# Kernel tuning notes

Measured on AMD Instinct MI355X. Metric: run time of the kernel, lower is better.

The kernel has to match this reference:

```python
import jax, jax.numpy as jnp
import numpy as np

jax.config.update("jax_enable_x64", True)

B, N, M_EQ, D_INEQ = 64, 128, 32, 64
RHO = 1.0
THRES = 1e-5
MAX_ITERS = 5000  # safety cap (original loops until relative objective change <= 1e-5)


def setup_inputs() -> dict:
    key = jax.random.key(0)
    kL, kq, kG, kA, kx0, ks = jax.random.split(key, 6)
    L = jax.random.normal(kL, (B, N, N))
    Q = jnp.einsum('bij,bkj->bik', L, L) / N + jnp.eye(N)  # SPD, well-conditioned
    q = jax.random.normal(kq, (B, N))
    G = jax.random.normal(kG, (B, D_INEQ, N))
    A = jax.random.normal(kA, (B, M_EQ, N))
    x0 = jax.random.normal(kx0, (B, N))
    slack = jax.random.uniform(ks, (B, D_INEQ)) + 0.1
    h = jnp.einsum('bdn,bn->bd', G, x0) + slack  # strictly feasible ineq
    b = jnp.einsum('bmn,bn->bm', A, x0)          # feasible eq
    f32 = jnp.float32
    return {"Q": Q.astype(f32), "q": q.astype(f32), "G": G.astype(f32),
            "h": h.astype(f32), "A": A.astype(f32), "b": b.astype(f32)}


def _alt_diff_batch(Q, q, G, h, A, b):
    """Batched Alt-Diff ADMM QP solve; returns (x [B,n], dx/dq [B,n,n])."""
    Bb, n = q.shape
    d = h.shape[1]
    m = b.shape[1]
    dt = Q.dtype
    AtA = jnp.einsum('bmi,bmj->bij', A, A)
    GtG = jnp.einsum('bdi,bdj->bij', G, G)
    R = -jnp.linalg.inv(Q + RHO * AtA + RHO * GtG)
    ATb = RHO * jnp.einsum('bmn,bm->bn', A, b)
    GTh = RHO * jnp.einsum('bdn,bd->bn', G, h)
    eye = jnp.eye(n, dtype=dt)

    def obj(x):
        return 0.5 * jnp.einsum('bi,bij,bj->b', x, Q, x) + jnp.einsum('bi,bi->b', q, x)

    init = dict(
        xk=jnp.zeros((Bb, n), dt), sk=jnp.zeros((Bb, d), dt),
        lamb=jnp.zeros((Bb, m), dt), nu=jnp.zeros((Bb, d), dt),
        dxk=jnp.zeros((Bb, n, n), dt), dsk=jnp.zeros((Bb, d, n), dt),
        dlamb=jnp.zeros((Bb, m, n), dt), dnu=jnp.zeros((Bb, d, n), dt),
        res_prev=jnp.full((Bb,), 1000.0, dt),   # res = [1000, -100] init
        res_cur=jnp.full((Bb,), -100.0, dt),
        done=jnp.zeros((Bb,), bool),
        it=jnp.zeros((), jnp.int32),
    )

    def cond(s):
        return jnp.logical_and(jnp.any(~s["done"]), s["it"] < MAX_ITERS)

    def body(s):
        xk = jnp.einsum('bij,bj->bi', R,
                        q + jnp.einsum('bmn,bm->bn', A, s["lamb"])
                          + jnp.einsum('bdn,bd->bn', G, s["nu"]) - ATb
                          + RHO * jnp.einsum('bdn,bd->bn', G, s["sk"]) - GTh)
        dxk = jnp.einsum('bij,bjk->bik', R,
                         eye + jnp.einsum('bmn,bmk->bnk', A, s["dlamb"])
                             + jnp.einsum('bdn,bdk->bnk', G, s["dnu"])
                             + RHO * jnp.einsum('bdn,bdk->bnk', G, s["dsk"]))
        Gx = jnp.einsum('bdn,bn->bd', G, xk)
        sk = jax.nn.relu(-(1.0 / RHO) * s["nu"] - (Gx - h))
        sgn = (sk > 0).astype(dt)  # sgn applied to already-relu'd sk, as in source
        dsk = (-1.0 / RHO) * sgn[:, :, None] * (s["dnu"] + RHO * jnp.einsum('bdn,bnk->bdk', G, dxk))
        lamb = s["lamb"] + RHO * (jnp.einsum('bmn,bn->bm', A, xk) - b)
        dlamb = s["dlamb"] + RHO * jnp.einsum('bmn,bnk->bmk', A, dxk)
        nu = s["nu"] + RHO * (Gx + sk - h)
        dnu = s["dnu"] + RHO * (jnp.einsum('bdn,bnk->bdk', G, dxk) + dsk)
        res_new = obj(xk)

        keep = s["done"]

        def sel(old, new):
            mask = keep.reshape((-1,) + (1,) * (new.ndim - 1))
            return jnp.where(mask, old, new)

        res_prev = jnp.where(keep, s["res_prev"], s["res_cur"])
        res_cur = jnp.where(keep, s["res_cur"], res_new)
        done = keep | (jnp.abs((res_cur - res_prev) / res_prev) <= THRES)
        return dict(
            xk=sel(s["xk"], xk), sk=sel(s["sk"], sk),
            lamb=sel(s["lamb"], lamb), nu=sel(s["nu"], nu),
            dxk=sel(s["dxk"], dxk), dsk=sel(s["dsk"], dsk),
            dlamb=sel(s["dlamb"], dlamb), dnu=sel(s["dnu"], dnu),
            res_prev=res_prev, res_cur=res_cur, done=done, it=s["it"] + 1,
        )

    final = jax.lax.while_loop(cond, body, init)
    return final["xk"], final["dxk"]


def reference(Q, q, G, h, A, b):
    out_dtype = q.dtype
    f64 = jnp.float64
    x, _dx = _alt_diff_batch(Q.astype(f64), q.astype(f64), G.astype(f64),
                             h.astype(f64), A.astype(f64), b.astype(f64))
    return x.astype(out_dtype)
```

## Files before the change

### kernel.cpp

```cpp
#include <hip/hip_runtime.h>

#define NN 128
#define ME 32
#define DI 64
#define NZ 96
#define ROWD 130
#define MAXIT 5000

#define OFF_UN 16640
#define ROWB  (OFF_UN)
#define COLB  (OFF_UN + 256)
#define FPLO  (2*OFF_UN)
#define FPHI  (2*OFF_UN + 512)
#define TV0   (OFF_UN + 384)
#define TV1   (OFF_UN + 512)
#define FLG   (OFF_UN + 544)
#define YBUF  (OFF_UN)
#define KBUF  (OFF_UN + 1536)
#define CPART (OFF_UN + 1024)
#define VP    (OFF_UN + 1280)
#define BASEV (OFF_UN + 1792)
#define QBV   (OFF_UN + 1888)
#define FPART (OFF_UN + 1024)
#define RHSV  (OFF_UN + 1280)
#define XPART (OFF_UN + 1408)
#define CB    (OFF_UN + 2688)
#define QBUF  (OFF_UN + 2816)
#define V1    (OFF_UN + 2944)
#define V2    (OFF_UN + 3072)
#define HB    (OFF_UN + 3200)
#define BB    (OFF_UN + 3264)
#define CST   (OFF_UN + 3296)
#define ZBF   (OFF_UN + 3304)
#define LDS_DBL (OFF_UN + 3400)

typedef __attribute__((ext_vector_type(2))) float f32x2;

__device__ __forceinline__ float rlf(float v, int lane) {
  return __uint_as_float((unsigned)__builtin_amdgcn_readlane((int)__float_as_uint(v), lane));
}
__device__ __forceinline__ f32x2 fma2(f32x2 a, f32x2 b, f32x2 c) {
  return __builtin_elementwise_fma(a, b, c);
}

__global__ __launch_bounds__(256, 1) void altdiff_kernel(
    const float* __restrict__ Qg, const float* __restrict__ qg,
    const float* __restrict__ Gg, const float* __restrict__ hg,
    const float* __restrict__ Ag, const float* __restrict__ bg,
    float* __restrict__ out)
{
  extern __shared__ double ldsd[];
  float* const ldsf = (float*)ldsd;

  const int bidx = blockIdx.x;
  const int tid  = threadIdx.x;
  const int w    = tid >> 6;
  const int l    = tid & 63;
  const int lm   = l & 31;
  const int ia   = tid & 127;
  const int hh   = tid >> 7;

  const float* Qb = Qg + (size_t)bidx * NN * NN;
  const float* Ab = Ag + (size_t)bidx * ME * NN;
  const float* Gb = Gg + (size_t)bidx * DI * NN;
  const float* qb = qg + (size_t)bidx * NN;
  const float* hb = hg + (size_t)bidx * DI;
  const float* bv = bg + (size_t)bidx * ME;

  if (tid < DI) ldsd[HB + tid] = (double)hb[tid];
  else if (tid < DI + ME) ldsd[BB + tid - DI] = (double)bv[tid - DI];
  if (tid >= 128) ldsd[QBUF + tid - 128] = (double)qb[tid - 128];

  const int r = tid >> 4, c = tid & 15;
  double acc[8][8];

  {
    const float4* Q4 = (const float4*)Qb;
#pragma unroll
    for (int rr = 0; rr < 8; ++rr) {
      float4 q0 = Q4[((8*r+rr) << 5) + 2*c];
      float4 q1 = Q4[((8*r+rr) << 5) + 2*c + 1];
      acc[rr][0]=(double)q0.x; acc[rr][1]=(double)q0.y; acc[rr][2]=(double)q0.z; acc[rr][3]=(double)q0.w;
      acc[rr][4]=(double)q1.x; acc[rr][5]=(double)q1.y; acc[rr][6]=(double)q1.z; acc[rr][7]=(double)q1.w;
    }
    const float4* A4 = (const float4*)Ab;
    for (int m = 0; m < ME; ++m) {
      float4 u0 = A4[(m << 5) + 2*r], u1 = A4[(m << 5) + 2*r + 1];
      float4 v0 = A4[(m << 5) + 2*c], v1 = A4[(m << 5) + 2*c + 1];
      double uu[8] = {(double)u0.x,(double)u0.y,(double)u0.z,(double)u0.w,
                      (double)u1.x,(double)u1.y,(double)u1.z,(double)u1.w};
      double vv[8] = {(double)v0.x,(double)v0.y,(double)v0.z,(double)v0.w,
                      (double)v1.x,(double)v1.y,(double)v1.z,(double)v1.w};
#pragma unroll
      for (int rr = 0; rr < 8; ++rr)
#pragma unroll
        for (int cc = 0; cc < 8; ++cc)
          acc[rr][cc] = fma(uu[rr], vv[cc], acc[rr][cc]);
    }
    const float4* G4 = (const float4*)Gb;
    for (int d = 0; d < DI; ++d) {
      float4 u0 = G4[(d << 5) + 2*r], u1 = G4[(d << 5) + 2*r + 1];
      float4 v0 = G4[(d << 5) + 2*c], v1 = G4[(d << 5) + 2*c + 1];
      double uu[8] = {(double)u0.x,(double)u0.y,(double)u0.z,(double)u0.w,
                      (double)u1.x,(double)u1.y,(double)u1.z,(double)u1.w};
      double vv[8] = {(double)v0.x,(double)v0.y,(double)v0.z,(double)v0.w,
                      (double)v1.x,(double)v1.y,(double)v1.z,(double)v1.w};
#pragma unroll
      for (int rr = 0; rr < 8; ++rr)
#pragma unroll
        for (int cc = 0; cc < 8; ++cc)
          acc[rr][cc] = fma(uu[rr], vv[cc], acc[rr][cc]);
    }
  }

  {
    if (r == 0) {
#pragma unroll
      for (int cc = 0; cc < 8; ++cc) ldsd[ROWB + 8*c + cc] = acc[0][cc];
    }
    if (c == 0) {
#pragma unroll
      for (int rr = 0; rr < 8; ++rr) ldsd[COLB + 8*r + rr] = acc[rr][0];
    }
    __syncthreads();
    for (int k = 0; k < NN; ++k) {
      const int pb = (k & 1) << 7;
      const int krt = k >> 3, kcl = k & 7;
      double rowk[8], colv[8];
#pragma unroll
      for (int cc = 0; cc < 8; ++cc) rowk[cc] = ldsd[ROWB + pb + 8*c + cc];
#pragma unroll
      for (int rr = 0; rr < 8; ++rr) colv[rr] = ldsd[COLB + pb + 8*r + rr];
      const double dkk  = ldsd[ROWB + pb + k];
      const double rcpd = 1.0 / dkk;
      double rdv[8];
#pragma unroll
      for (int cc = 0; cc < 8; ++cc) rdv[cc] = rowk[cc] * rcpd;
      const bool pivR = (r == krt), pivC = (c == krt);
#pragma unroll
      for (int rr = 0; rr < 8; ++rr) {
        const double cv = colv[rr] * rcpd;
        const bool pr = pivR && (rr == kcl);
#pragma unroll
        for (int cc = 0; cc < 8; ++cc) {
          double gen = fma(-cv, rowk[cc], acc[rr][cc]);
          acc[rr][cc] = pr ? rdv[cc] : gen;
        }
      }
      if (pivC) {
#pragma unroll
        for (int cc = 0; cc < 8; ++cc) if (cc == kcl) {
#pragma unroll
          for (int rr = 0; rr < 8; ++rr) {
            const bool pr2 = pivR && (rr == kcl);
            acc[rr][cc] = pr2 ? -rcpd : colv[rr] * rcpd;
          }
        }
      }
      if (k < NN - 1) {
        const int pb2 = ((k + 1) & 1) << 7;
        const int krt2 = (k + 1) >> 3, kcl2 = (k + 1) & 7;
        if (r == krt2) {
#pragma unroll
          for (int rr = 0; rr < 8; ++rr) if (rr == kcl2) {
#pragma unroll
            for (int cc = 0; cc < 8; ++cc) ldsd[ROWB + pb2 + 8*c + cc] = acc[rr][cc];
          }
        }
        if (c == krt2) {
#pragma unroll
          for (int cc = 0; cc < 8; ++cc) if (cc == kcl2) {
#pragma unroll
            for (int rr = 0; rr < 8; ++rr) ldsd[COLB + pb2 + 8*r + rr] = acc[rr][cc];
          }
        }
      }
      __syncthreads();
    }
#pragma unroll
    for (int rr = 0; rr < 8; ++rr) {
      double2* dst = (double2*)(ldsd + (8*r+rr)*ROWD + 8*c);
#pragma unroll
      for (int t = 0; t < 4; ++t) dst[t] = make_double2(acc[rr][2*t], acc[rr][2*t+1]);
    }
  }
  __syncthreads();

  f32x2 Kp[12], Kp2[12];
  for (int blk = 0; blk < 8; ++blk) {
    {
      const float* gp[6];
#pragma unroll
      for (int jj = 0; jj < 6; ++jj) {
        int it = 12*blk + 6*hh + jj;
        gp[jj] = (it < DI) ? (Gb + it*NN) : (Ab + (it - DI)*NN);
      }
      double a2[6] = {0,0,0,0,0,0};
#pragma unroll 4
      for (int t = 0; t < NN; ++t) {
        double rv = ldsd[t*ROWD + ia];
#pragma unroll
        for (int jj = 0; jj < 6; ++jj)
          a2[jj] = fma(rv, (double)gp[jj][t], a2[jj]);
      }
      double2* yst = (double2*)(ldsd + YBUF + ia*12 + 6*hh);
#pragma unroll
      for (int p = 0; p < 3; ++p) yst[p] = make_double2(a2[2*p], a2[2*p+1]);
    }
    __syncthreads();
    {
      const int r2 = (ia < NZ) ? ia : 0;
      const float* brow = (r2 < DI) ? (Gb + r2*NN) : (Ab + (r2 - DI)*NN);
      double a2[6] = {0,0,0,0,0,0};
#pragma unroll 4
      for (int t = 0; t < NN; ++t) {
        double bvv = (double)brow[t];
        const double2* yr = (const double2*)(ldsd + YBUF + t*12 + 6*hh);
        double2 y0 = yr[0], y1 = yr[1], y2 = yr[2];
        a2[0] = fma(bvv, y0.x, a2[0]); a2[1] = fma(bvv, y0.y, a2[1]);
        a2[2] = fma(bvv, y1.x, a2[2]); a2[3] = fma(bvv, y1.y, a2[3]);
        a2[4] = fma(bvv, y2.x, a2[4]); a2[5] = fma(bvv, y2.y, a2[5]);
      }
      if (ia < NZ) {
#pragma unroll
        for (int jj = 0; jj < 6; ++jj) ldsd[KBUF + (6*hh + jj)*NZ + ia] = a2[jj];
      }
    }
    __syncthreads();
    if (w == (blk >> 1)) {
      if ((blk & 1) == 0) {
#pragma unroll
        for (int p = 0; p < 6; ++p) {
          Kp [p].x = (float)ldsd[KBUF + (2*p  )*NZ + l];
          Kp [p].y = (float)ldsd[KBUF + (2*p+1)*NZ + l];
          Kp2[p].x = (float)ldsd[KBUF + (2*p  )*NZ + 64 + lm];
          Kp2[p].y = (float)ldsd[KBUF + (2*p+1)*NZ + 64 + lm];
        }
      } else {
#pragma unroll
        for (int p = 0; p < 6; ++p) {
          Kp [6+p].x = (float)ldsd[KBUF + (2*p  )*NZ + l];
          Kp [6+p].y = (float)ldsd[KBUF + (2*p+1)*NZ + l];
          Kp2[6+p].x = (float)ldsd[KBUF + (2*p  )*NZ + 64 + lm];
          Kp2[6+p].y = (float)ldsd[KBUF + (2*p+1)*NZ + 64 + lm];
        }
      }
    }
    __syncthreads();
  }

  {
    double s = 0;
#pragma unroll 8
    for (int jc = 0; jc < 48; ++jc) {
      int j = 48*hh + jc;
      double coef = (j < DI) ? ldsd[HB + j] : ldsd[BB + j - DI];
      const float* src = (j < DI) ? (Gb + j*NN) : (Ab + (j - DI)*NN);
      s = fma(-(double)src[ia], coef, s);
    }
    ldsd[CPART + hh*128 + ia] = s;
  }
  __syncthreads();
  if (tid < NN) ldsd[CB + tid] = ldsd[QBUF + tid] + ldsd[CPART + tid] + ldsd[CPART + 128 + tid];
  __syncthreads();

  {
    double a = 0, b2 = 0;
#pragma unroll 4
    for (int tt = 0; tt < 64; ++tt) {
      int t = 64*hh + tt;
      double rv = ldsd[t*ROWD + ia];
      a  = fma(rv, ldsd[CB + t], a);
      b2 = fma(rv, ldsd[QBUF + t], b2);
    }
    ldsd[VP + hh*128 + ia] = a;
    ldsd[VP + 256 + hh*128 + ia] = b2;
  }
  __syncthreads();
  if (tid < NN) {
    ldsd[V1 + tid] = ldsd[VP + tid] + ldsd[VP + 128 + tid];
    ldsd[V2 + tid] = ldsd[VP + 256 + tid] + ldsd[VP + 384 + tid];
  }
  __syncthreads();

  {
    const int r2 = (ia < NZ) ? ia : 0;
    const float* brow = (r2 < DI) ? (Gb + r2*NN) : (Ab + (r2 - DI)*NN);
    const int voff = hh ? V2 : V1;
    double s = 0;
#pragma unroll 4
    for (int t = 0; t < NN; ++t) s = fma((double)brow[t], ldsd[voff + t], s);
    if (ia < NZ) ldsd[(hh ? QBV : BASEV) + ia] = s;
  }
  if (w == 0) {
    double pc = ldsd[V1+l]*ldsd[CB+l]   + ldsd[V1+64+l]*ldsd[CB+64+l];
    double pq = ldsd[V1+l]*ldsd[QBUF+l] + ldsd[V1+64+l]*ldsd[QBUF+64+l];
#pragma unroll
    for (int off = 32; off >= 1; off >>= 1) { pc += __shfl_xor(pc, off); pq += __shfl_xor(pq, off); }
    if (l == 0) { ldsd[CST] = pc; ldsd[CST+1] = pq; }
  }
  __syncthreads();

  const double h_r   = ldsd[HB + l];
  const double b_r   = ldsd[BB + lm];
  const double baseA = ldsd[BASEV + l];
  const double baseB = ldsd[BASEV + 64 + lm];
  const double qvA   = ldsd[QBV + l];
  const double qvB   = ldsd[QBV + 64 + lm];
  const double S_uc  = ldsd[CST], S_qu = ldsd[CST + 1];
  double nu = 0.0, lam = 0.0;
  double zlo = 0.0, zhi = 0.0;
  double zAlo = 0.0, zAhi = 0.0, zBlo = 0.0, zBhi = 0.0, zClo = 0.0, zChi = 0.0;
  double res_prev = 1000.0, res_cur = -100.0;

  {
    ldsf[FPLO + 4*l + (w ^ (l & 3))] = 0.f;
    if (l < 32) ldsf[FPHI + 4*lm + (w ^ (lm & 3))] = 0.f;
    if (tid == 0) { ldsd[FLG] = 0.0; ldsd[FLG + 1] = 0.0; }
  }

  for (int it = 0; it < MAXIT + 3; ++it) {
    __syncthreads();
    const int pf  = (it & 1) << 8;
    const int phf = (it & 1) << 7;
    const int bprev = (it + 1) & 1;
    double fl = ldsd[FLG + bprev];
    float4 plo = {0.f, 0.f, 0.f, 0.f}, phi4 = {0.f, 0.f, 0.f, 0.f};
    if (w != 3) plo  = *(const float4*)&ldsf[FPLO + pf  + 4*l];
    if (w >= 2) phi4 = *(const float4*)&ldsf[FPHI + phf + 4*lm];
    double t1v[16];
    if (w == 1) {
      const double2* tp = (const double2*)(ldsd + TV1 + bprev*16);
#pragma unroll
      for (int u = 0; u < 8; ++u) { double2 v = tp[u]; t1v[2*u] = v.x; t1v[2*u+1] = v.y; }
    }
    double a40 = 0, a41 = 0, a42 = 0, a43 = 0;
    if (w == 3) {
      const int g = l & 15;
      const double* tb = ldsd + TV0 + bprev*64;
      a40 = tb[g]; a41 = tb[g + 16]; a42 = tb[g + 32]; a43 = tb[g + 48];
    }
    double ylo = 0.0, yhi = 0.0;
    if (w != 3) ylo = (double)((plo.x + plo.y) + (plo.z + plo.w)) + baseA;
    if (w >= 2) yhi = (double)((phi4.x + phi4.y) + (phi4.z + phi4.w)) + baseB;
    if (it >= 3 && fl != 0.0) break;
    if (w == 2) { zClo = zBlo; zChi = zBhi; zBlo = zAlo; zBhi = zAhi; zAlo = zlo; zAhi = zhi; }
    if (it < MAXIT) {
      float zflo = 0.f, zfhi = 0.f;
      if (w != 3) {
        double t  = (h_r - nu) - ylo;
        double sk = fmax(t, 0.0);
        nu  = sk - t;
        zlo = nu + sk;
        zflo = (float)zlo;
      }
      if (w >= 2) {
        lam = lam + yhi - b_r;
        zhi = lam;
        zfhi = (float)zhi;
      }
      if (w == 2) {
        double tv = fma(qvA, zAlo, -0.5*(zAlo*(baseA + ylo) + ylo*ylo));
        tv += (l < 32) ? fma(qvB, zAhi, -0.5*(zAhi*(baseB + yhi) + yhi*yhi)) : 0.0;
        ldsd[TV0 + (it & 1)*64 + l] = tv;
      }
      f32x2 A0 = {0.f, 0.f}, A1 = A0, B0 = A0, B1 = A0;
      if (w == 0) {
#pragma unroll
        for (int p = 0; p < 12; p += 2) {
          f32x2 z0 = {rlf(zflo, 2*p),     rlf(zflo, 2*p + 1)};
          A0 = fma2(Kp[p],   z0, A0); B0 = fma2(Kp2[p],   z0, B0);
          f32x2 z1 = {rlf(zflo, 2*p + 2), rlf(zflo, 2*p + 3)};
          A1 = fma2(Kp[p+1], z1, A1); B1 = fma2(Kp2[p+1], z1, B1);
        }
      } else if (w == 1) {
#pragma unroll
        for (int p = 0; p < 12; p += 2) {
          f32x2 z0 = {rlf(zflo, 24 + 2*p),     rlf(zflo, 24 + 2*p + 1)};
          A0 = fma2(Kp[p],   z0, A0); B0 = fma2(Kp2[p],   z0, B0);
          f32x2 z1 = {rlf(zflo, 24 + 2*p + 2), rlf(zflo, 24 + 2*p + 3)};
          A1 = fma2(Kp[p+1], z1, A1); B1 = fma2(Kp2[p+1], z1, B1);
        }
      } else if (w == 2) {
#pragma unroll
        for (int p = 0; p < 8; p += 2) {
          f32x2 z0 = {rlf(zflo, 48 + 2*p),     rlf(zflo, 48 + 2*p + 1)};
          A0 = fma2(Kp[p],   z0, A0); B0 = fma2(Kp2[p],   z0, B0);
          f32x2 z1 = {rlf(zflo, 48 + 2*p + 2), rlf(zflo, 48 + 2*p + 3)};
          A1 = fma2(Kp[p+1], z1, A1); B1 = fma2(Kp2[p+1], z1, B1);
        }
#pragma unroll
        for (int p = 8; p < 12; p += 2) {
          f32x2 z0 = {rlf(zfhi, 2*(p-8)),     rlf(zfhi, 2*(p-8) + 1)};
          A0 = fma2(Kp[p],   z0, A0); B0 = fma2(Kp2[p],   z0, B0);
          f32x2 z1 = {rlf(zfhi, 2*(p-7)),     rlf(zfhi, 2*(p-7) + 1)};
          A1 = fma2(Kp[p+1], z1, A1); B1 = fma2(Kp2[p+1], z1, B1);
        }
      } else {
#pragma unroll
        for (int p = 0; p < 12; p += 2) {
          f32x2 z0 = {rlf(zfhi, 8 + 2*p),     rlf(zfhi, 8 + 2*p + 1)};
          A0 = fma2(Kp[p],   z0, A0); B0 = fma2(Kp2[p],   z0, B0);
          f32x2 z1 = {rlf(zfhi, 8 + 2*p + 2), rlf(zfhi, 8 + 2*p + 3)};
          A1 = fma2(Kp[p+1], z1, A1); B1 = fma2(Kp2[p+1], z1, B1);
        }
      }
      f32x2 As = A0 + A1, Bs = B0 + B1;
      float pa0 = As.x + As.y;
      float pa1 = Bs.x + Bs.y;
      ldsf[FPLO + (pf ^ 256) + 4*l + (w ^ (l & 3))] = pa0;
      if (l < 32) ldsf[FPHI + (phf ^ 128) + 4*lm + (w ^ (lm & 3))] = pa1;
    }
    if (w == 3 && l < 16 && it >= 1 && it <= MAXIT)
      ldsd[TV1 + (it & 1)*16 + l] = (a40 + a41) + (a42 + a43);
    if (w == 1 && it >= 2 && it <= MAXIT + 1) {
      double s1 = ((t1v[0] + t1v[1]) + (t1v[2] + t1v[3])) + ((t1v[4] + t1v[5]) + (t1v[6] + t1v[7]));
      double s2 = ((t1v[8] + t1v[9]) + (t1v[10] + t1v[11])) + ((t1v[12] + t1v[13]) + (t1v[14] + t1v[15]));
      double obj = (s1 + s2) - 0.5*S_uc + S_qu;
      res_prev = res_cur; res_cur = obj;
      if (l == 0)
        ldsd[FLG + (it & 1)] = (fabs(res_cur - res_prev) <= 1e-5 * fabs(res_prev)) ? 1.0 : 0.0;
    }
  }

  if (w == 2) {
    ldsd[ZBF + l] = zClo;
    if (l < 32) ldsd[ZBF + 64 + l] = zChi;
  }
  __syncthreads();
  {
    double s = 0;
#pragma unroll 8
    for (int jc = 0; jc < 48; ++jc) {
      int j = 48*hh + jc;
      double zj = ldsd[ZBF + j];
      const float* src = (j < DI) ? (Gb + j*NN) : (Ab + (j - DI)*NN);
      s = fma((double)src[ia], zj, s);
    }
    ldsd[FPART + hh*128 + ia] = s;
  }
  __syncthreads();
  if (tid < NN) ldsd[RHSV + tid] = ldsd[CB + tid] + ldsd[FPART + tid] + ldsd[FPART + 128 + tid];
  __syncthreads();
  {
    double s = 0;
#pragma unroll 4
    for (int tt = 0; tt < 64; ++tt) {
      int t = 64*hh + tt;
      s = fma(ldsd[t*ROWD + ia], ldsd[RHSV + t], s);
    }
    ldsd[XPART + hh*128 + ia] = s;
  }
  __syncthreads();
  if (tid < NN)
    out[(size_t)bidx * NN + tid] = (float)(ldsd[XPART + tid] + ldsd[XPART + 128 + tid]);
}

extern "C" void kernel_launch(void* const* d_in, const int* in_sizes, int n_in,
                              void* d_out, int out_size, void* d_ws, size_t ws_size,
                              hipStream_t stream) {
  (void)in_sizes; (void)n_in; (void)out_size; (void)d_ws; (void)ws_size;
  const float* Q = (const float*)d_in[0];
  const float* q = (const float*)d_in[1];
  const float* G = (const float*)d_in[2];
  const float* h = (const float*)d_in[3];
  const float* A = (const float*)d_in[4];
  const float* b = (const float*)d_in[5];
  float* out = (float*)d_out;
  const size_t lds_bytes = (size_t)LDS_DBL * sizeof(double);
  altdiff_kernel<<<dim3(64), dim3(256), lds_bytes, stream>>>(Q, q, G, h, A, b, out);
}
```

Baseline: 661.0 us.

## Rebalance per-wave matvec columns and simplify ADMM dual update algebra

Redistributes the 96 z-columns of the K matvec so waves take 24/16/30/26 columns, instead of each wave taking 24, to even out per-wave work alongside the scalar updates. The nu/sk recurrence is rewritten algebraically: z = |t| and nu-carrying becomes hnb = (h - base) + min(t,0), which cuts dependent double ops on the critical path. The objective-term work is split between waves 0 and 3. The partial-sum layout changes from swizzled float4 to strided scalar loads. This risks numerical divergence in the rewritten recurrence and adds more LDS load instructions.

Result: slower. 686.0 us (+3.8%).

```diff
diff --git a/kernel.cpp b/kernel.cpp
--- a/kernel.cpp
+++ b/kernel.cpp
@@ -10,11 +10,12 @@
 #define OFF_UN 16640
 #define ROWB  (OFF_UN)
 #define COLB  (OFF_UN + 256)
-#define FPLO  (2*OFF_UN)
-#define FPHI  (2*OFF_UN + 512)
-#define TV0   (OFF_UN + 384)
-#define TV1   (OFF_UN + 512)
-#define FLG   (OFF_UN + 544)
+#define FPLO_F (2*(OFF_UN))
+#define FPHI_F (2*(OFF_UN) + 512)
+#define TV0L  (OFF_UN + 384)
+#define TV0H  (OFF_UN + 512)
+#define TV1   (OFF_UN + 576)
+#define FLG   (OFF_UN + 608)
 #define YBUF  (OFF_UN)
 #define KBUF  (OFF_UN + 1536)
 #define CPART (OFF_UN + 1024)
@@ -43,6 +44,24 @@
   return __builtin_elementwise_fma(a, b, c);
 }
 
+#define CPYRANGE(LBASE, KBASE, CNT)                                        \
+  _Pragma("unroll") for (int j = 0; j < (CNT); ++j) {                      \
+    const int lj = (LBASE) + j, kc = (KBASE) + j;                          \
+    float va = (float)ldsd[KBUF + kc*NZ + l];                              \
+    float vb = (float)ldsd[KBUF + kc*NZ + 64 + lm];                        \
+    if ((lj & 1) == 0) { Kp[lj>>1].x = va; Kp2[lj>>1].x = vb; }            \
+    else               { Kp[lj>>1].y = va; Kp2[lj>>1].y = vb; }            \
+  }
+
+#define MV2(PA, ZS, L0) {                                                  \
+    f32x2 z0 = { rlf(ZS, L0), rlf(ZS, (L0)+1) };                           \
+    A0 = fma2(Kp[PA], z0, A0); B0 = fma2(Kp2[PA], z0, B0);                 \
+    f32x2 z1 = { rlf(ZS, (L0)+2), rlf(ZS, (L0)+3) };                       \
+    A1 = fma2(Kp[(PA)+1], z1, A1); B1 = fma2(Kp2[(PA)+1], z1, B1); }
+#define MV1(PA, ZS, L0) {                                                  \
+    f32x2 z0 = { rlf(ZS, L0), rlf(ZS, (L0)+1) };                           \
+    A0 = fma2(Kp[PA], z0, A0); B0 = fma2(Kp2[PA], z0, B0); }
+
 __global__ __launch_bounds__(256, 1) void altdiff_kernel(
     const float* __restrict__ Qg, const float* __restrict__ qg,
     const float* __restrict__ Gg, const float* __restrict__ hg,
@@ -186,7 +205,7 @@
   }
   __syncthreads();
 
-  f32x2 Kp[12], Kp2[12];
+  f32x2 Kp[15], Kp2[15];
   for (int blk = 0; blk < 8; ++blk) {
     {
       const float* gp[6];
@@ -227,24 +246,20 @@
       }
     }
     __syncthreads();
-    if (w == (blk >> 1)) {
-      if ((blk & 1) == 0) {
-#pragma unroll
-        for (int p = 0; p < 6; ++p) {
-          Kp [p].x = (float)ldsd[KBUF + (2*p  )*NZ + l];
-          Kp [p].y = (float)ldsd[KBUF + (2*p+1)*NZ + l];
-          Kp2[p].x = (float)ldsd[KBUF + (2*p  )*NZ + 64 + lm];
-          Kp2[p].y = (float)ldsd[KBUF + (2*p+1)*NZ + 64 + lm];
-        }
-      } else {
-#pragma unroll
-        for (int p = 0; p < 6; ++p) {
-          Kp [6+p].x = (float)ldsd[KBUF + (2*p  )*NZ + l];
-          Kp [6+p].y = (float)ldsd[KBUF + (2*p+1)*NZ + l];
-          Kp2[6+p].x = (float)ldsd[KBUF + (2*p  )*NZ + 64 + lm];
-          Kp2[6+p].y = (float)ldsd[KBUF + (2*p+1)*NZ + 64 + lm];
-        }
-      }
+    if (w == 0) {
+      if (blk == 0)      { CPYRANGE(0,  0, 12) }
+      else if (blk == 1) { CPYRANGE(12, 0, 12) }
+    } else if (w == 1) {
+      if (blk == 2)      { CPYRANGE(0,  0, 12) }
+      else if (blk == 3) { CPYRANGE(12, 0, 4) }
+    } else if (w == 2) {
+      if (blk == 3)      { CPYRANGE(0,  4, 8) }
+      else if (blk == 4) { CPYRANGE(8,  0, 12) }
+      else if (blk == 5) { CPYRANGE(20, 0, 10) }
+    } else {
+      if (blk == 5)      { CPYRANGE(0,  10, 2) }
+      else if (blk == 6) { CPYRANGE(2,  0, 12) }
+      else if (blk == 7) { CPYRANGE(14, 0, 12) }
     }
     __syncthreads();
   }
@@ -301,132 +316,117 @@
   }
   __syncthreads();
 
-  const double h_r   = ldsd[HB + l];
-  const double b_r   = ldsd[BB + lm];
   const double baseA = ldsd[BASEV + l];
   const double baseB = ldsd[BASEV + 64 + lm];
   const double qvA   = ldsd[QBV + l];
   const double qvB   = ldsd[QBV + 64 + lm];
+  const double hb2   = ldsd[HB + l] - baseA;
+  const double bb2   = baseB - ldsd[BB + lm];
   const double S_uc  = ldsd[CST], S_qu = ldsd[CST + 1];
-  double nu = 0.0, lam = 0.0;
+  double hnb = hb2, lb = bb2;
   double zlo = 0.0, zhi = 0.0;
   double zAlo = 0.0, zAhi = 0.0, zBlo = 0.0, zBhi = 0.0, zClo = 0.0, zChi = 0.0;
   double res_prev = 1000.0, res_cur = -100.0;
 
   {
-    ldsf[FPLO + 4*l + (w ^ (l & 3))] = 0.f;
-    if (l < 32) ldsf[FPHI + 4*lm + (w ^ (lm & 3))] = 0.f;
+    ldsf[FPLO_F + (w << 6) + l] = 0.f;
+    if (l < 32) ldsf[FPHI_F + (w << 5) + l] = 0.f;
     if (tid == 0) { ldsd[FLG] = 0.0; ldsd[FLG + 1] = 0.0; }
   }
 
   for (int it = 0; it < MAXIT + 3; ++it) {
     __syncthreads();
-    const int pf  = (it & 1) << 8;
-    const int phf = (it & 1) << 7;
+    const int buf = it & 1, nbuf = buf ^ 1;
     const int bprev = (it + 1) & 1;
     double fl = ldsd[FLG + bprev];
-    float4 plo = {0.f, 0.f, 0.f, 0.f}, phi4 = {0.f, 0.f, 0.f, 0.f};
-    if (w != 3) plo  = *(const float4*)&ldsf[FPLO + pf  + 4*l];
-    if (w >= 2) phi4 = *(const float4*)&ldsf[FPHI + phf + 4*lm];
+    float p0 = 0.f, p1 = 0.f, p2 = 0.f, p3 = 0.f, q0 = 0.f, q1 = 0.f, q2 = 0.f, q3 = 0.f;
+    if (w != 3) {
+      const int fb = FPLO_F + (buf << 8) + l;
+      p0 = ldsf[fb]; p1 = ldsf[fb + 64]; p2 = ldsf[fb + 128]; p3 = ldsf[fb + 192];
+    }
+    if (w >= 2) {
+      const int fb = FPHI_F + (buf << 7) + lm;
+      q0 = ldsf[fb]; q1 = ldsf[fb + 32]; q2 = ldsf[fb + 64]; q3 = ldsf[fb + 96];
+    }
     double t1v[16];
     if (w == 1) {
       const double2* tp = (const double2*)(ldsd + TV1 + bprev*16);
 #pragma unroll
       for (int u = 0; u < 8; ++u) { double2 v = tp[u]; t1v[2*u] = v.x; t1v[2*u+1] = v.y; }
     }
-    double a40 = 0, a41 = 0, a42 = 0, a43 = 0;
+    double a40 = 0, a41 = 0, a42 = 0, a43 = 0, a44 = 0, a45 = 0;
     if (w == 3) {
       const int g = l & 15;
-      const double* tb = ldsd + TV0 + bprev*64;
-      a40 = tb[g]; a41 = tb[g + 16]; a42 = tb[g + 32]; a43 = tb[g + 48];
-    }
-    double ylo = 0.0, yhi = 0.0;
-    if (w != 3) ylo = (double)((plo.x + plo.y) + (plo.z + plo.w)) + baseA;
-    if (w >= 2) yhi = (double)((phi4.x + phi4.y) + (phi4.z + phi4.w)) + baseB;
+      const double* tl = ldsd + TV0L + bprev*64;
+      const double* th = ldsd + TV0H + bprev*32;
+      a40 = tl[g]; a41 = tl[g + 16]; a42 = tl[g + 32]; a43 = tl[g + 48];
+      a44 = th[g]; a45 = th[g + 16];
+    }
+    double slo = 0.0, t = 0.0, shi = 0.0, lamn = 0.0;
+    float zflo = 0.f, zfhi = 0.f;
+    if (w != 3) {
+      float s = (p0 + p1) + (p2 + p3);
+      slo = (double)s; t = hnb - slo;
+      zflo = (float)fabs(t);
+    }
+    if (w >= 2) {
+      float sh = (q0 + q1) + (q2 + q3);
+      shi = (double)sh; lamn = lb + shi;
+      zfhi = (float)lamn;
+    }
     if (it >= 3 && fl != 0.0) break;
-    if (w == 2) { zClo = zBlo; zChi = zBhi; zBlo = zAlo; zBhi = zAhi; zAlo = zlo; zAhi = zhi; }
+    if (w == 0) { zClo = zBlo; zBlo = zAlo; zAlo = zlo; }
+    if (w == 3) { zChi = zBhi; zBhi = zAhi; zAhi = zhi; }
     if (it < MAXIT) {
-      float zflo = 0.f, zfhi = 0.f;
-      if (w != 3) {
-        double t  = (h_r - nu) - ylo;
-        double sk = fmax(t, 0.0);
-        nu  = sk - t;
-        zlo = nu + sk;
-        zflo = (float)zlo;
-      }
-      if (w >= 2) {
-        lam = lam + yhi - b_r;
-        zhi = lam;
-        zfhi = (float)zhi;
-      }
-      if (w == 2) {
-        double tv = fma(qvA, zAlo, -0.5*(zAlo*(baseA + ylo) + ylo*ylo));
-        tv += (l < 32) ? fma(qvB, zAhi, -0.5*(zAhi*(baseB + yhi) + yhi*yhi)) : 0.0;
-        ldsd[TV0 + (it & 1)*64 + l] = tv;
-      }
+      if (w == 0) zlo = fabs(t);
+      if (w != 3) hnb = hb2 + fmin(t, 0.0);
+      if (w == 3) zhi = lamn;
+      if (w >= 2) lb = lamn + bb2;
       f32x2 A0 = {0.f, 0.f}, A1 = A0, B0 = A0, B1 = A0;
       if (w == 0) {
-#pragma unroll
-        for (int p = 0; p < 12; p += 2) {
-          f32x2 z0 = {rlf(zflo, 2*p),     rlf(zflo, 2*p + 1)};
-          A0 = fma2(Kp[p],   z0, A0); B0 = fma2(Kp2[p],   z0, B0);
-          f32x2 z1 = {rlf(zflo, 2*p + 2), rlf(zflo, 2*p + 3)};
-          A1 = fma2(Kp[p+1], z1, A1); B1 = fma2(Kp2[p+1], z1, B1);
-        }
+        MV2(0, zflo, 0)  MV2(2, zflo, 4)  MV2(4, zflo, 8)
+        MV2(6, zflo, 12) MV2(8, zflo, 16) MV2(10, zflo, 20)
       } else if (w == 1) {
-#pragma unroll
-        for (int p = 0; p < 12; p += 2) {
-          f32x2 z0 = {rlf(zflo, 24 + 2*p),     rlf(zflo, 24 + 2*p + 1)};
-          A0 = fma2(Kp[p],   z0, A0); B0 = fma2(Kp2[p],   z0, B0);
-          f32x2 z1 = {rlf(zflo, 24 + 2*p + 2), rlf(zflo, 24 + 2*p + 3)};
-          A1 = fma2(Kp[p+1], z1, A1); B1 = fma2(Kp2[p+1], z1, B1);
-        }
+        MV2(0, zflo, 24) MV2(2, zflo, 28) MV2(4, zflo, 32) MV2(6, zflo, 36)
       } else if (w == 2) {
-#pragma unroll
-        for (int p = 0; p < 8; p += 2) {
-          f32x2 z0 = {rlf(zflo, 48 + 2*p),     rlf(zflo, 48 + 2*p + 1)};
-          A0 = fma2(Kp[p],   z0, A0); B0 = fma2(Kp2[p],   z0, B0);
-          f32x2 z1 = {rlf(zflo, 48 + 2*p + 2), rlf(zflo, 48 + 2*p + 3)};
-          A1 = fma2(Kp[p+1], z1, A1); B1 = fma2(Kp2[p+1], z1, B1);
-        }
-#pragma unroll
-        for (int p = 8; p < 12; p += 2) {
-          f32x2 z0 = {rlf(zfhi, 2*(p-8)),     rlf(zfhi, 2*(p-8) + 1)};
-          A0 = fma2(Kp[p],   z0, A0); B0 = fma2(Kp2[p],   z0, B0);
-          f32x2 z1 = {rlf(zfhi, 2*(p-7)),     rlf(zfhi, 2*(p-7) + 1)};
-          A1 = fma2(Kp[p+1], z1, A1); B1 = fma2(Kp2[p+1], z1, B1);
-        }
+        MV2(0, zflo, 40) MV2(2, zflo, 44) MV2(4, zflo, 48)
+        MV2(6, zflo, 52) MV2(8, zflo, 56) MV2(10, zflo, 60)
+        MV2(12, zfhi, 0) MV1(14, zfhi, 4)
       } else {
-#pragma unroll
-        for (int p = 0; p < 12; p += 2) {
-          f32x2 z0 = {rlf(zfhi, 8 + 2*p),     rlf(zfhi, 8 + 2*p + 1)};
-          A0 = fma2(Kp[p],   z0, A0); B0 = fma2(Kp2[p],   z0, B0);
-          f32x2 z1 = {rlf(zfhi, 8 + 2*p + 2), rlf(zfhi, 8 + 2*p + 3)};
-          A1 = fma2(Kp[p+1], z1, A1); B1 = fma2(Kp2[p+1], z1, B1);
-        }
+        MV2(0, zfhi, 6)  MV2(2, zfhi, 10) MV2(4, zfhi, 14)
+        MV2(6, zfhi, 18) MV2(8, zfhi, 22) MV2(10, zfhi, 26)
+        MV1(12, zfhi, 30)
       }
       f32x2 As = A0 + A1, Bs = B0 + B1;
       float pa0 = As.x + As.y;
       float pa1 = Bs.x + Bs.y;
-      ldsf[FPLO + (pf ^ 256) + 4*l + (w ^ (l & 3))] = pa0;
-      if (l < 32) ldsf[FPHI + (phf ^ 128) + 4*lm + (w ^ (lm & 3))] = pa1;
+      ldsf[FPLO_F + (nbuf << 8) + (w << 6) + l] = pa0;
+      if (l < 32) ldsf[FPHI_F + (nbuf << 7) + (w << 5) + l] = pa1;
+      if (w == 0) {
+        double yfull = slo + baseA;
+        double tvl = fma(qvA, zAlo, -0.5*(zAlo*(baseA + yfull) + yfull*yfull));
+        ldsd[TV0L + buf*64 + l] = tvl;
+      }
+      if (w == 3) {
+        double yfB = shi + baseB;
+        double tvh = fma(qvB, zAhi, -0.5*(zAhi*(baseB + yfB) + yfB*yfB));
+        if (l < 32) ldsd[TV0H + buf*32 + l] = tvh;
+      }
     }
     if (w == 3 && l < 16 && it >= 1 && it <= MAXIT)
-      ldsd[TV1 + (it & 1)*16 + l] = (a40 + a41) + (a42 + a43);
+      ldsd[TV1 + buf*16 + l] = ((a40 + a41) + (a42 + a43)) + (a44 + a45);
     if (w == 1 && it >= 2 && it <= MAXIT + 1) {
       double s1 = ((t1v[0] + t1v[1]) + (t1v[2] + t1v[3])) + ((t1v[4] + t1v[5]) + (t1v[6] + t1v[7]));
       double s2 = ((t1v[8] + t1v[9]) + (t1v[10] + t1v[11])) + ((t1v[12] + t1v[13]) + (t1v[14] + t1v[15]));
       double obj = (s1 + s2) - 0.5*S_uc + S_qu;
       res_prev = res_cur; res_cur = obj;
       if (l == 0)
-        ldsd[FLG + (it & 1)] = (fabs(res_cur - res_prev) <= 1e-5 * fabs(res_prev)) ? 1.0 : 0.0;
-    }
-  }
-
-  if (w == 2) {
-    ldsd[ZBF + l] = zClo;
-    if (l < 32) ldsd[ZBF + 64 + l] = zChi;
-  }
+        ldsd[FLG + buf] = (fabs(res_cur - res_prev) <= 1e-5 * fabs(res_prev)) ? 1.0 : 0.0;
+    }
+  }
+
+  if (w == 0) ldsd[ZBF + l] = zClo;
+  if (w == 3 && l < 32) ldsd[ZBF + 64 + l] = zChi;
   __syncthreads();
   {
     double s = 0;
```
